# Kernel optimization log

Hardware: AMD Instinct MI355X
Metric: run time of the kernel (lower is better)

Reference implementation:

```python
import jax, jax.numpy as jnp
import numpy as np

B, T, C, H = 8, 2048, 1024, 64

def setup_inputs() -> dict:
    key = jax.random.key(0)
    k1, k2, k3, k4 = jax.random.split(key, 4)
    x = jax.random.normal(k1, (B, T, C), dtype=jnp.float32)
    # torch nn.Linear default init ~ U(-1/sqrt(in), 1/sqrt(in)); scale kept small for stability
    s = 1.0 / np.sqrt(C)
    Wq = jax.random.uniform(k2, (C, H), dtype=jnp.float32, minval=-s, maxval=s)
    Wk = jax.random.uniform(k3, (C, H), dtype=jnp.float32, minval=-s, maxval=s)
    Wv = jax.random.uniform(k4, (C, H), dtype=jnp.float32, minval=-s, maxval=s)
    return {"x": x, "Wq": Wq, "Wk": Wk, "Wv": Wv}

def reference(x, Wq, Wk, Wv):
    # x: [B,T,C]; Wq/Wk/Wv: [C,H] (equivalent to torch Linear weight transposed)
    Q = jnp.einsum('btc,ch->bth', x, Wq)
    K = jnp.einsum('btc,ch->bth', x, Wk)
    V = jnp.einsum('btc,ch->bth', x, Wv)
    H_ = Q.shape[-1]
    scale = 1.0 / jnp.sqrt(jnp.asarray(H_, dtype=Q.dtype))
    w = jnp.einsum('bqh,bkh->bqk', Q, K) * scale  # [B,T,T]
    T_ = x.shape[1]
    causal = jnp.tril(jnp.ones((T_, T_), dtype=bool))
    w = jnp.where(causal, w, -jnp.inf)
    w = jax.nn.softmax(w, axis=-1)
    out = jnp.einsum('bqk,bkh->bqh', w, V)  # [B,T,H]
    return out
```

## Files before the change

### kernel.cpp

```cpp
#include <hip/hip_runtime.h>
#include <math.h>

#define Bb 8
#define Tt 2048
#define Cc 1024
#define Hh 64
#define BT (Bb * Tt)
#define SLOG2E 0.18033688011112042f

typedef __attribute__((ext_vector_type(8))) short short8;
typedef __attribute__((ext_vector_type(4))) float floatx4;

__device__ inline unsigned short f2bf(float f) {
  unsigned int u = __builtin_bit_cast(unsigned int, f);
  u += 0x7fff + ((u >> 16) & 1);
  return (unsigned short)(u >> 16);
}
__device__ inline float bf2f(unsigned short u) {
  unsigned int x = ((unsigned int)u) << 16;
  return __builtin_bit_cast(float, x);
}


__global__ __launch_bounds__(256) void wconv2(
    const float* __restrict__ Wq, const float* __restrict__ Wk,
    const float* __restrict__ Wv, unsigned short* __restrict__ WTf) {
  int bid = blockIdx.x;
  int w = bid >> 5;
  int kc = bid & 31;
  const float* __restrict__ W = (w == 0) ? Wq : (w == 1 ? Wk : Wv);
  int t = threadIdx.x;
  int hg = t >> 6, quad = (t >> 4) & 3, lrow = t & 15;
  int g = w * 4 + hg;
  int h = hg * 16 + lrow;
  unsigned short tmp[8];
#pragma unroll
  for (int j = 0; j < 8; ++j)
    tmp[j] = f2bf(W[(size_t)(kc * 32 + quad * 8 + j) * Hh + h]);
  unsigned short* dst = &WTf[((size_t)(g * 32 + kc) * 64 + quad * 16 + lrow) * 8];
  *(ushort4*)dst = make_ushort4(tmp[0], tmp[1], tmp[2], tmp[3]);
  *(ushort4*)(dst + 4) = make_ushort4(tmp[4], tmp[5], tmp[6], tmp[7]);
}

__global__ __launch_bounds__(256) void qkv7(
    const float* __restrict__ x, const unsigned short* __restrict__ WTf,
    unsigned short* __restrict__ Qf, unsigned short* __restrict__ Kf,
    unsigned short* __restrict__ Vf) {
  __shared__ __align__(16) unsigned short smem7[6656];

  int mt = blockIdx.x;
  int t = threadIdx.x;
  int wv = t >> 6, lane = t & 63;
  int lrow = lane & 15, quad = lane >> 4;

  floatx4 acc[2][3];
#pragma unroll
  for (int g2 = 0; g2 < 2; ++g2)
#pragma unroll
    for (int j = 0; j < 3; ++j)
#pragma unroll
      for (int r = 0; r < 4; ++r) acc[g2][j][r] = 0.f;

  int srow = t >> 3, scg = t & 7;
  int skc2 = scg >> 2, squad = scg & 3;
  int sslot = ((srow >> 4) * 2 + skc2) * 64 + squad * 16 +
              (((srow & 15) + squad + 4 * skc2) & 15);
  const float* xp = x + (size_t)(mt * 32 + srow) * Cc + scg * 8;

  int aslot[2][2];
#pragma unroll
  for (int g2 = 0; g2 < 2; ++g2)
#pragma unroll
    for (int kc2 = 0; kc2 < 2; ++kc2)
      aslot[g2][kc2] = ((g2 * 2 + kc2) * 64 + quad * 16 +
                        ((lrow + quad + 4 * kc2) & 15)) * 8;

  const unsigned short* wbase[3];
#pragma unroll
  for (int j = 0; j < 3; ++j)
    wbase[j] = WTf + (size_t)(wv * 3 + j) * 32 * 512 + lane * 8;

  {
    float4 v0 = *(const float4*)xp;
    float4 v1 = *(const float4*)(xp + 4);
    short8 a;
    a[0] = (short)f2bf(v0.x); a[1] = (short)f2bf(v0.y);
    a[2] = (short)f2bf(v0.z); a[3] = (short)f2bf(v0.w);
    a[4] = (short)f2bf(v1.x); a[5] = (short)f2bf(v1.y);
    a[6] = (short)f2bf(v1.z); a[7] = (short)f2bf(v1.w);
    *(short8*)&smem7[sslot * 8] = a;
  }
  __syncthreads();

  for (int kk = 0; kk < 16; ++kk) {
    int cur = kk & 1;
    float4 v0, v1;
    if (kk < 15) {
      v0 = *(const float4*)(xp + (kk + 1) * 64);
      v1 = *(const float4*)(xp + (kk + 1) * 64 + 4);
    }
    short8 bf[3][2];
    int kg = kk * 2;
#pragma unroll
    for (int j = 0; j < 3; ++j)
#pragma unroll
      for (int kc2 = 0; kc2 < 2; ++kc2)
        bf[j][kc2] = *(const short8*)(wbase[j] + (size_t)(kg + kc2) * 512);
    short8 af[2][2];
#pragma unroll
    for (int g2 = 0; g2 < 2; ++g2)
#pragma unroll
      for (int kc2 = 0; kc2 < 2; ++kc2)
        af[g2][kc2] = *(const short8*)&smem7[cur * 2048 + aslot[g2][kc2]];
#pragma unroll
    for (int g2 = 0; g2 < 2; ++g2)
#pragma unroll
      for (int j = 0; j < 3; ++j) {
        acc[g2][j] = __builtin_amdgcn_mfma_f32_16x16x32_bf16(af[g2][0], bf[j][0], acc[g2][j], 0, 0, 0);
        acc[g2][j] = __builtin_amdgcn_mfma_f32_16x16x32_bf16(af[g2][1], bf[j][1], acc[g2][j], 0, 0, 0);
      }
    if (kk < 15) {
      short8 a;
      a[0] = (short)f2bf(v0.x); a[1] = (short)f2bf(v0.y);
      a[2] = (short)f2bf(v0.z); a[3] = (short)f2bf(v0.w);
      a[4] = (short)f2bf(v1.x); a[5] = (short)f2bf(v1.y);
      a[6] = (short)f2bf(v1.z); a[7] = (short)f2bf(v1.w);
      *(short8*)&smem7[(1 - cur) * 2048 + sslot * 8] = a;
      __syncthreads();
    }
  }

  __syncthreads();
#pragma unroll
  for (int g2 = 0; g2 < 2; ++g2)
#pragma unroll
    for (int j = 0; j < 3; ++j) {
      int col = (wv * 3 + j) * 16 + lrow;
#pragma unroll
      for (int r = 0; r < 4; ++r)
        smem7[(g2 * 16 + quad * 4 + r) * 208 + col] = f2bf(acc[g2][j][r]);
    }
  __syncthreads();
#pragma unroll
  for (int fi = 0; fi < 3; ++fi) {
    int idx = fi * 256 + t;
    if (idx < 512) {
      int which = idx >> 8;
      int sub = idx & 255;
      int g2k = sub >> 6, lane_s = sub & 63;
      int g2_ = g2k >> 1, kc_ = g2k & 1;
      int tokrow = g2_ * 16 + (lane_s & 15);
      int hbase = which * 64 + kc_ * 32 + (lane_s >> 4) * 8;
      short8 v = *(const short8*)&smem7[tokrow * 208 + hbase];
      unsigned short* dstf = which ? Kf : Qf;
      *(short8*)&dstf[((size_t)(mt * 2 + g2_) * 2 + kc_) * 512 + lane_s * 8] = v;
    } else {
      int sub = idx - 512;
      int hs = sub >> 6, lane_s = sub & 63;
      int hcol = 128 + hs * 16 + (lane_s & 15);
      int tok0 = (lane_s >> 4) * 8;
      unsigned short tmp[8];
#pragma unroll
      for (int jj = 0; jj < 8; ++jj) tmp[jj] = smem7[(tok0 + jj) * 208 + hcol];
      unsigned short* dv = &Vf[((size_t)(mt * 4 + hs)) * 512 + lane_s * 8];
      *(ushort4*)dv = make_ushort4(tmp[0], tmp[1], tmp[2], tmp[3]);
      *(ushort4*)(dv + 4) = make_ushort4(tmp[4], tmp[5], tmp[6], tmp[7]);
    }
  }
}

__global__ __launch_bounds__(512) void attn6(
    const unsigned short* __restrict__ Qf, const unsigned short* __restrict__ Kf,
    const unsigned short* __restrict__ Vf, float* __restrict__ out) {
  __shared__ __align__(16) unsigned char smem[33 * 1024];
  unsigned short* Pall = (unsigned short*)smem;
  unsigned short* Ocomb = (unsigned short*)smem;
  float* Lcomb = (float*)(smem + 32768);

  int bid = blockIdx.x;
  int b = bid >> 5;
  int j = bid & 31;
  int t = threadIdx.x;
  int wv = t >> 6, lane = t & 63;
  int lrow = lane & 15, quad = lane >> 4;

  unsigned short* Pw = Pall + wv * 2048;

  short8 ones;
#pragma unroll
  for (int i = 0; i < 8; ++i) ones[i] = (short)0x3F80;

  for (int half = 0; half < 2; ++half) {
    int qt = half ? (63 - j) : j;
    int q0 = qt * 32;
    int nkt = (qt >> 1) + 1;
    int qtile16 = b * 128 + qt * 2;

    short8 aq[2][2];
#pragma unroll
    for (int qs = 0; qs < 2; ++qs)
#pragma unroll
      for (int kc = 0; kc < 2; ++kc)
        aq[qs][kc] = *(const short8*)
            &Qf[((size_t)(qtile16 + qs) * 2 + kc) * 512 + lane * 8];

    floatx4 acc_o[2][4];
    floatx4 acc_l[2];
#pragma unroll
    for (int qs = 0; qs < 2; ++qs) {
#pragma unroll
      for (int r = 0; r < 4; ++r) acc_l[qs][r] = 0.f;
#pragma unroll
      for (int hs = 0; hs < 4; ++hs)
#pragma unroll
        for (int r = 0; r < 4; ++r) acc_o[qs][hs][r] = 0.f;
    }

    for (int kt = wv; kt < nkt; kt += 8) {
      int ktile16 = b * 128 + kt * 4;
      int ktile32 = b * 64 + kt * 2;
      short8 kf[4][2], vf[4][2];
#pragma unroll
      for (int sn = 0; sn < 4; ++sn)
#pragma unroll
        for (int kc = 0; kc < 2; ++kc)
          kf[sn][kc] = *(const short8*)
              &Kf[((size_t)(ktile16 + sn) * 2 + kc) * 512 + lane * 8];
#pragma unroll
      for (int hs = 0; hs < 4; ++hs)
#pragma unroll
        for (int kc = 0; kc < 2; ++kc)
          vf[hs][kc] = *(const short8*)
              &Vf[((size_t)(ktile32 + kc) * 4 + hs) * 512 + lane * 8];

      floatx4 s[2][4];
#pragma unroll
      for (int qs = 0; qs < 2; ++qs)
#pragma unroll
        for (int sn = 0; sn < 4; ++sn) {
          floatx4 z;
#pragma unroll
          for (int r = 0; r < 4; ++r) z[r] = 0.f;
          z = __builtin_amdgcn_mfma_f32_16x16x32_bf16(aq[qs][0], kf[sn][0], z, 0, 0, 0);
          z = __builtin_amdgcn_mfma_f32_16x16x32_bf16(aq[qs][1], kf[sn][1], z, 0, 0, 0);
          s[qs][sn] = z;
        }

      bool diag = (kt == nkt - 1);
#pragma unroll
      for (int qs = 0; qs < 2; ++qs)
#pragma unroll
        for (int sn = 0; sn < 4; ++sn) {
          int k5 = (sn & 1) * 16 + lrow;
          int slot = qs * 2 + (sn >> 1);
          int rlbase = (k5 >> 3) * 16;
#pragma unroll
          for (int r = 0; r < 4; ++r) {
            float v = s[qs][sn][r] * SLOG2E;
            if (diag) {
              int gk = kt * 64 + sn * 16 + lrow;
              int gq = q0 + qs * 16 + quad * 4 + r;
              if (gk > gq) v = -INFINITY;
            }
            float p = exp2f(v);
            Pw[slot * 512 + (rlbase + quad * 4 + r) * 8 + (k5 & 7)] = f2bf(p);
          }
        }

      short8 ap[2][2];
#pragma unroll
      for (int qs = 0; qs < 2; ++qs)
#pragma unroll
        for (int kc = 0; kc < 2; ++kc)
          ap[qs][kc] = *(const short8*)&Pw[(qs * 2 + kc) * 512 + lane * 8];

#pragma unroll
      for (int qs = 0; qs < 2; ++qs) {
        acc_l[qs] = __builtin_amdgcn_mfma_f32_16x16x32_bf16(ap[qs][0], ones, acc_l[qs], 0, 0, 0);
        acc_l[qs] = __builtin_amdgcn_mfma_f32_16x16x32_bf16(ap[qs][1], ones, acc_l[qs], 0, 0, 0);
#pragma unroll
        for (int hs = 0; hs < 4; ++hs) {
          acc_o[qs][hs] = __builtin_amdgcn_mfma_f32_16x16x32_bf16(ap[qs][0], vf[hs][0], acc_o[qs][hs], 0, 0, 0);
          acc_o[qs][hs] = __builtin_amdgcn_mfma_f32_16x16x32_bf16(ap[qs][1], vf[hs][1], acc_o[qs][hs], 0, 0, 0);
        }
      }
    }

#pragma unroll
    for (int qs = 0; qs < 2; ++qs)
#pragma unroll
      for (int hs = 0; hs < 4; ++hs) {
        int s8 = qs * 4 + hs;
        *(ushort4*)&Ocomb[((wv * 8 + s8) * 64 + lane) * 4] =
            make_ushort4(f2bf(acc_o[qs][hs][0]), f2bf(acc_o[qs][hs][1]),
                         f2bf(acc_o[qs][hs][2]), f2bf(acc_o[qs][hs][3]));
      }
    if (lrow == 0) {
#pragma unroll
      for (int qs = 0; qs < 2; ++qs)
#pragma unroll
        for (int r = 0; r < 4; ++r)
          Lcomb[wv * 32 + qs * 16 + quad * 4 + r] = acc_l[qs][r];
    }
    __syncthreads();

    {
      int qsub = wv >> 2, hs = wv & 3;
      float o[4] = {0.f, 0.f, 0.f, 0.f};
#pragma unroll
      for (int w = 0; w < 8; ++w) {
        ushort4 pk = *(const ushort4*)&Ocomb[((w * 8 + wv) * 64 + lane) * 4];
        o[0] += bf2f(pk.x); o[1] += bf2f(pk.y);
        o[2] += bf2f(pk.z); o[3] += bf2f(pk.w);
      }
#pragma unroll
      for (int r = 0; r < 4; ++r) {
        float lv = 0.f;
#pragma unroll
        for (int w = 0; w < 8; ++w)
          lv += Lcomb[w * 32 + qsub * 16 + quad * 4 + r];
        int row = q0 + qsub * 16 + quad * 4 + r;
        out[(size_t)(b * Tt + row) * Hh + hs * 16 + lrow] = o[r] / lv;
      }
    }
    __syncthreads();
  }
}

extern "C" void kernel_launch(void* const* d_in, const int* in_sizes, int n_in,
                              void* d_out, int out_size, void* d_ws, size_t ws_size,
                              hipStream_t stream) {
  const float* x = (const float*)d_in[0];
  const float* Wq = (const float*)d_in[1];
  const float* Wk = (const float*)d_in[2];
  const float* Wv = (const float*)d_in[3];
  float* out = (float*)d_out;

  unsigned short* WTf = (unsigned short*)d_ws;
  unsigned short* Qf = WTf + 192 * 1024;
  unsigned short* Kf = Qf + (size_t)(BT / 16) * 2 * 512;
  unsigned short* Vf = Kf + (size_t)(BT / 16) * 2 * 512;

  wconv2<<<dim3(96), dim3(256), 0, stream>>>(Wq, Wk, Wv, WTf);
  qkv7<<<dim3(512), dim3(256), 0, stream>>>(x, WTf, Qf, Kf, Vf);
  attn6<<<dim3(256), dim3(512), 0, stream>>>(Qf, Kf, Vf, out);
}
```

Baseline: 132.4 us.

## Fuse weight conversion, QKV projection and attention into one cooperative kernel

Replaces three separate kernel launches with a single cooperative kernel that uses grid-wide syncs between weight conversion, QKV projection and attention. The projection stage is retiled to 64 tokens per 512-thread block so 256 blocks cover the work. The intent is to remove launch gaps and tail effects between the stages. In exchange it adds the cost of grid.sync and requires all 256 blocks to be co-resident; the old three-launch path is kept as a fallback if the cooperative launch fails.

```diff
diff --git a/kernel.cpp b/kernel.cpp
--- a/kernel.cpp
+++ b/kernel.cpp
@@ -1,5 +1,8 @@
 #include <hip/hip_runtime.h>
+#include <hip/hip_cooperative_groups.h>
 #include <math.h>
+
+namespace cg = cooperative_groups;
 
 #define Bb 8
 #define Tt 2048
@@ -21,6 +24,318 @@
   return __builtin_bit_cast(float, x);
 }
 
+
+__global__ __launch_bounds__(512) void fused(
+    const float* __restrict__ x,
+    const float* __restrict__ Wq, const float* __restrict__ Wk,
+    const float* __restrict__ Wv,
+    unsigned short* __restrict__ WTf,
+    unsigned short* __restrict__ Qf, unsigned short* __restrict__ Kf,
+    unsigned short* __restrict__ Vf, float* __restrict__ out) {
+  __shared__ __align__(16) unsigned char smemF[34304];
+  cg::grid_group grid = cg::this_grid();
+
+  int bid = blockIdx.x;
+  int t = threadIdx.x;
+  int wv = t >> 6, lane = t & 63;
+  int lrow = lane & 15, quad = lane >> 4;
+
+  if (bid < 48) {
+    int unit = bid * 2 + (t >> 8);
+    int tt = t & 255;
+    int w = unit >> 5;
+    int kc = unit & 31;
+    const float* __restrict__ W = (w == 0) ? Wq : (w == 1 ? Wk : Wv);
+    int hg = tt >> 6, q_ = (tt >> 4) & 3, lr_ = tt & 15;
+    int g = w * 4 + hg;
+    int h = hg * 16 + lr_;
+    unsigned short tmp[8];
+#pragma unroll
+    for (int j = 0; j < 8; ++j)
+      tmp[j] = f2bf(W[(size_t)(kc * 32 + q_ * 8 + j) * Hh + h]);
+    unsigned short* dst = &WTf[((size_t)(g * 32 + kc) * 64 + q_ * 16 + lr_) * 8];
+    *(ushort4*)dst = make_ushort4(tmp[0], tmp[1], tmp[2], tmp[3]);
+    *(ushort4*)(dst + 4) = make_ushort4(tmp[4], tmp[5], tmp[6], tmp[7]);
+  }
+  grid.sync();
+
+  {
+    unsigned short* Af = (unsigned short*)smemF;
+    int mt = bid;
+    int wm = wv & 1;
+    int wq = wv >> 1;
+
+    floatx4 acc[2][3];
+#pragma unroll
+    for (int i = 0; i < 2; ++i)
+#pragma unroll
+      for (int j = 0; j < 3; ++j)
+#pragma unroll
+        for (int r = 0; r < 4; ++r) acc[i][j][r] = 0.f;
+
+    int srow = t >> 3, scg = t & 7;
+    int skc2 = scg >> 2, squad = scg & 3;
+    int sslot = ((srow >> 4) * 2 + skc2) * 512 +
+                (squad * 16 + (((srow & 15) + squad + 4 * skc2) & 15)) * 8;
+    const float* xp = x + (size_t)(mt * 64 + srow) * Cc + scg * 8;
+
+    int aslot[2][2];
+#pragma unroll
+    for (int i = 0; i < 2; ++i)
+#pragma unroll
+      for (int kc2 = 0; kc2 < 2; ++kc2) {
+        int ms = wm * 2 + i;
+        aslot[i][kc2] = ((ms * 2 + kc2) * 512 +
+                         (quad * 16 + ((lrow + quad + 4 * kc2) & 15)) * 8);
+      }
+
+    const unsigned short* wbase[3];
+#pragma unroll
+    for (int j = 0; j < 3; ++j)
+      wbase[j] = WTf + (size_t)(wq * 3 + j) * 32 * 512 + lane * 8;
+
+    {
+      float4 v0 = *(const float4*)xp;
+      float4 v1 = *(const float4*)(xp + 4);
+      short8 a;
+      a[0] = (short)f2bf(v0.x); a[1] = (short)f2bf(v0.y);
+      a[2] = (short)f2bf(v0.z); a[3] = (short)f2bf(v0.w);
+      a[4] = (short)f2bf(v1.x); a[5] = (short)f2bf(v1.y);
+      a[6] = (short)f2bf(v1.z); a[7] = (short)f2bf(v1.w);
+      *(short8*)&Af[sslot] = a;
+    }
+    __syncthreads();
+
+    for (int kk = 0; kk < 16; ++kk) {
+      int cur = kk & 1;
+      float4 v0, v1;
+      if (kk < 15) {
+        v0 = *(const float4*)(xp + (kk + 1) * 64);
+        v1 = *(const float4*)(xp + (kk + 1) * 64 + 4);
+      }
+      short8 bfr[3][2];
+      int kg = kk * 2;
+#pragma unroll
+      for (int j = 0; j < 3; ++j)
+#pragma unroll
+        for (int kc2 = 0; kc2 < 2; ++kc2)
+          bfr[j][kc2] = *(const short8*)(wbase[j] + (size_t)(kg + kc2) * 512);
+      short8 af[2][2];
+#pragma unroll
+      for (int i = 0; i < 2; ++i)
+#pragma unroll
+        for (int kc2 = 0; kc2 < 2; ++kc2)
+          af[i][kc2] = *(const short8*)&Af[cur * 4096 + aslot[i][kc2]];
+#pragma unroll
+      for (int i = 0; i < 2; ++i)
+#pragma unroll
+        for (int j = 0; j < 3; ++j) {
+          acc[i][j] = __builtin_amdgcn_mfma_f32_16x16x32_bf16(af[i][0], bfr[j][0], acc[i][j], 0, 0, 0);
+          acc[i][j] = __builtin_amdgcn_mfma_f32_16x16x32_bf16(af[i][1], bfr[j][1], acc[i][j], 0, 0, 0);
+        }
+      if (kk < 15) {
+        short8 a;
+        a[0] = (short)f2bf(v0.x); a[1] = (short)f2bf(v0.y);
+        a[2] = (short)f2bf(v0.z); a[3] = (short)f2bf(v0.w);
+        a[4] = (short)f2bf(v1.x); a[5] = (short)f2bf(v1.y);
+        a[6] = (short)f2bf(v1.z); a[7] = (short)f2bf(v1.w);
+        *(short8*)&Af[(1 - cur) * 4096 + sslot] = a;
+        __syncthreads();
+      }
+    }
+
+    __syncthreads();
+    unsigned short* Dt = (unsigned short*)smemF;
+#pragma unroll
+    for (int i = 0; i < 2; ++i)
+#pragma unroll
+      for (int j = 0; j < 3; ++j) {
+        int col = (wq * 3 + j) * 16 + lrow;
+        int rowb = (wm * 2 + i) * 16 + quad * 4;
+#pragma unroll
+        for (int r = 0; r < 4; ++r)
+          Dt[(rowb + r) * 208 + col] = f2bf(acc[i][j][r]);
+      }
+    __syncthreads();
+#pragma unroll
+    for (int fi = 0; fi < 3; ++fi) {
+      int idx = fi * 512 + t;
+      int tile = idx >> 6, lane_s = idx & 63;
+      if (tile < 16) {
+        int which = tile >> 3;
+        int sub = tile & 7;
+        int g2 = sub >> 1, kc = sub & 1;
+        int tokrow = g2 * 16 + (lane_s & 15);
+        int hbase = which * 64 + kc * 32 + (lane_s >> 4) * 8;
+        short8 v = *(const short8*)&Dt[tokrow * 208 + hbase];
+        unsigned short* dstf = which ? Kf : Qf;
+        *(short8*)&dstf[((size_t)(mt * 4 + g2) * 2 + kc) * 512 + lane_s * 8] = v;
+      } else {
+        int sub = tile - 16;
+        int t32 = sub >> 2, hs = sub & 3;
+        int hcol = 128 + hs * 16 + (lane_s & 15);
+        int tok0 = t32 * 32 + (lane_s >> 4) * 8;
+        unsigned short tmp[8];
+#pragma unroll
+        for (int jj = 0; jj < 8; ++jj) tmp[jj] = Dt[(tok0 + jj) * 208 + hcol];
+        unsigned short* dv = &Vf[((size_t)(mt * 2 + t32) * 4 + hs) * 512 + lane_s * 8];
+        *(ushort4*)dv = make_ushort4(tmp[0], tmp[1], tmp[2], tmp[3]);
+        *(ushort4*)(dv + 4) = make_ushort4(tmp[4], tmp[5], tmp[6], tmp[7]);
+      }
+    }
+  }
+  grid.sync();
+
+  {
+    unsigned short* Pall = (unsigned short*)smemF;
+    unsigned short* Ocomb = (unsigned short*)smemF;
+    float* Lcomb = (float*)(smemF + 32768);
+    unsigned short* Pw = Pall + wv * 2048;
+
+    int b = bid >> 5;
+    int j = bid & 31;
+
+    short8 ones;
+#pragma unroll
+    for (int i = 0; i < 8; ++i) ones[i] = (short)0x3F80;
+
+    for (int half = 0; half < 2; ++half) {
+      int qt = half ? (63 - j) : j;
+      int q0 = qt * 32;
+      int nkt = (qt >> 1) + 1;
+      int qtile16 = b * 128 + qt * 2;
+
+      short8 aq[2][2];
+#pragma unroll
+      for (int qs = 0; qs < 2; ++qs)
+#pragma unroll
+        for (int kc = 0; kc < 2; ++kc)
+          aq[qs][kc] = *(const short8*)
+              &Qf[((size_t)(qtile16 + qs) * 2 + kc) * 512 + lane * 8];
+
+      floatx4 acc_o[2][4];
+      floatx4 acc_l[2];
+#pragma unroll
+      for (int qs = 0; qs < 2; ++qs) {
+#pragma unroll
+        for (int r = 0; r < 4; ++r) acc_l[qs][r] = 0.f;
+#pragma unroll
+        for (int hs = 0; hs < 4; ++hs)
+#pragma unroll
+          for (int r = 0; r < 4; ++r) acc_o[qs][hs][r] = 0.f;
+      }
+
+      for (int kt = wv; kt < nkt; kt += 8) {
+        int ktile16 = b * 128 + kt * 4;
+        int ktile32 = b * 64 + kt * 2;
+        short8 kf[4][2], vf[4][2];
+#pragma unroll
+        for (int sn = 0; sn < 4; ++sn)
+#pragma unroll
+          for (int kc = 0; kc < 2; ++kc)
+            kf[sn][kc] = *(const short8*)
+                &Kf[((size_t)(ktile16 + sn) * 2 + kc) * 512 + lane * 8];
+#pragma unroll
+        for (int hs = 0; hs < 4; ++hs)
+#pragma unroll
+          for (int kc = 0; kc < 2; ++kc)
+            vf[hs][kc] = *(const short8*)
+                &Vf[((size_t)(ktile32 + kc) * 4 + hs) * 512 + lane * 8];
+
+        floatx4 s[2][4];
+#pragma unroll
+        for (int qs = 0; qs < 2; ++qs)
+#pragma unroll
+          for (int sn = 0; sn < 4; ++sn) {
+            floatx4 z;
+#pragma unroll
+            for (int r = 0; r < 4; ++r) z[r] = 0.f;
+            z = __builtin_amdgcn_mfma_f32_16x16x32_bf16(aq[qs][0], kf[sn][0], z, 0, 0, 0);
+            z = __builtin_amdgcn_mfma_f32_16x16x32_bf16(aq[qs][1], kf[sn][1], z, 0, 0, 0);
+            s[qs][sn] = z;
+          }
+
+        bool diag = (kt == nkt - 1);
+#pragma unroll
+        for (int qs = 0; qs < 2; ++qs)
+#pragma unroll
+          for (int sn = 0; sn < 4; ++sn) {
+            int k5 = (sn & 1) * 16 + lrow;
+            int slot = qs * 2 + (sn >> 1);
+            int rlbase = (k5 >> 3) * 16;
+#pragma unroll
+            for (int r = 0; r < 4; ++r) {
+              float v = s[qs][sn][r] * SLOG2E;
+              if (diag) {
+                int gk = kt * 64 + sn * 16 + lrow;
+                int gq = q0 + qs * 16 + quad * 4 + r;
+                if (gk > gq) v = -INFINITY;
+              }
+              float p = exp2f(v);
+              Pw[slot * 512 + (rlbase + quad * 4 + r) * 8 + (k5 & 7)] = f2bf(p);
+            }
+          }
+
+        short8 ap[2][2];
+#pragma unroll
+        for (int qs = 0; qs < 2; ++qs)
+#pragma unroll
+          for (int kc = 0; kc < 2; ++kc)
+            ap[qs][kc] = *(const short8*)&Pw[(qs * 2 + kc) * 512 + lane * 8];
+
+#pragma unroll
+        for (int qs = 0; qs < 2; ++qs) {
+          acc_l[qs] = __builtin_amdgcn_mfma_f32_16x16x32_bf16(ap[qs][0], ones, acc_l[qs], 0, 0, 0);
+          acc_l[qs] = __builtin_amdgcn_mfma_f32_16x16x32_bf16(ap[qs][1], ones, acc_l[qs], 0, 0, 0);
+#pragma unroll
+          for (int hs = 0; hs < 4; ++hs) {
+            acc_o[qs][hs] = __builtin_amdgcn_mfma_f32_16x16x32_bf16(ap[qs][0], vf[hs][0], acc_o[qs][hs], 0, 0, 0);
+            acc_o[qs][hs] = __builtin_amdgcn_mfma_f32_16x16x32_bf16(ap[qs][1], vf[hs][1], acc_o[qs][hs], 0, 0, 0);
+          }
+        }
+      }
+
+#pragma unroll
+      for (int qs = 0; qs < 2; ++qs)
+#pragma unroll
+        for (int hs = 0; hs < 4; ++hs) {
+          int s8 = qs * 4 + hs;
+          *(ushort4*)&Ocomb[((wv * 8 + s8) * 64 + lane) * 4] =
+              make_ushort4(f2bf(acc_o[qs][hs][0]), f2bf(acc_o[qs][hs][1]),
+                           f2bf(acc_o[qs][hs][2]), f2bf(acc_o[qs][hs][3]));
+        }
+      if (lrow == 0) {
+#pragma unroll
+        for (int qs = 0; qs < 2; ++qs)
+#pragma unroll
+          for (int r = 0; r < 4; ++r)
+            Lcomb[wv * 32 + qs * 16 + quad * 4 + r] = acc_l[qs][r];
+      }
+      __syncthreads();
+
+      {
+        int qsub = wv >> 2, hs = wv & 3;
+        float o[4] = {0.f, 0.f, 0.f, 0.f};
+#pragma unroll
+        for (int w = 0; w < 8; ++w) {
+          ushort4 pk = *(const ushort4*)&Ocomb[((w * 8 + wv) * 64 + lane) * 4];
+          o[0] += bf2f(pk.x); o[1] += bf2f(pk.y);
+          o[2] += bf2f(pk.z); o[3] += bf2f(pk.w);
+        }
+#pragma unroll
+        for (int r = 0; r < 4; ++r) {
+          float lv = 0.f;
+#pragma unroll
+          for (int w = 0; w < 8; ++w)
+            lv += Lcomb[w * 32 + qsub * 16 + quad * 4 + r];
+          int row = q0 + qsub * 16 + quad * 4 + r;
+          out[(size_t)(b * Tt + row) * Hh + hs * 16 + lrow] = o[r] / lv;
+        }
+      }
+      __syncthreads();
+    }
+  }
+}
 
 __global__ __launch_bounds__(256) void wconv2(
     const float* __restrict__ Wq, const float* __restrict__ Wk,
@@ -47,12 +362,10 @@
     unsigned short* __restrict__ Qf, unsigned short* __restrict__ Kf,
     unsigned short* __restrict__ Vf) {
   __shared__ __align__(16) unsigned short smem7[6656];
-
   int mt = blockIdx.x;
   int t = threadIdx.x;
   int wv = t >> 6, lane = t & 63;
   int lrow = lane & 15, quad = lane >> 4;
-
   floatx4 acc[2][3];
 #pragma unroll
   for (int g2 = 0; g2 < 2; ++g2)
@@ -60,13 +373,11 @@
     for (int j = 0; j < 3; ++j)
 #pragma unroll
       for (int r = 0; r < 4; ++r) acc[g2][j][r] = 0.f;
-
   int srow = t >> 3, scg = t & 7;
   int skc2 = scg >> 2, squad = scg & 3;
   int sslot = ((srow >> 4) * 2 + skc2) * 64 + squad * 16 +
               (((srow & 15) + squad + 4 * skc2) & 15);
   const float* xp = x + (size_t)(mt * 32 + srow) * Cc + scg * 8;
-
   int aslot[2][2];
 #pragma unroll
   for (int g2 = 0; g2 < 2; ++g2)
@@ -74,12 +385,10 @@
     for (int kc2 = 0; kc2 < 2; ++kc2)
       aslot[g2][kc2] = ((g2 * 2 + kc2) * 64 + quad * 16 +
                         ((lrow + quad + 4 * kc2) & 15)) * 8;
-
   const unsigned short* wbase[3];
 #pragma unroll
   for (int j = 0; j < 3; ++j)
     wbase[j] = WTf + (size_t)(wv * 3 + j) * 32 * 512 + lane * 8;
-
   {
     float4 v0 = *(const float4*)xp;
     float4 v1 = *(const float4*)(xp + 4);
@@ -91,7 +400,6 @@
     *(short8*)&smem7[sslot * 8] = a;
   }
   __syncthreads();
-
   for (int kk = 0; kk < 16; ++kk) {
     int cur = kk & 1;
     float4 v0, v1;
@@ -99,13 +407,13 @@
       v0 = *(const float4*)(xp + (kk + 1) * 64);
       v1 = *(const float4*)(xp + (kk + 1) * 64 + 4);
     }
-    short8 bf[3][2];
+    short8 bfr[3][2];
     int kg = kk * 2;
 #pragma unroll
     for (int j = 0; j < 3; ++j)
 #pragma unroll
       for (int kc2 = 0; kc2 < 2; ++kc2)
-        bf[j][kc2] = *(const short8*)(wbase[j] + (size_t)(kg + kc2) * 512);
+        bfr[j][kc2] = *(const short8*)(wbase[j] + (size_t)(kg + kc2) * 512);
     short8 af[2][2];
 #pragma unroll
     for (int g2 = 0; g2 < 2; ++g2)
@@ -116,8 +424,8 @@
     for (int g2 = 0; g2 < 2; ++g2)
 #pragma unroll
       for (int j = 0; j < 3; ++j) {
-        acc[g2][j] = __builtin_amdgcn_mfma_f32_16x16x32_bf16(af[g2][0], bf[j][0], acc[g2][j], 0, 0, 0);
-        acc[g2][j] = __builtin_amdgcn_mfma_f32_16x16x32_bf16(af[g2][1], bf[j][1], acc[g2][j], 0, 0, 0);
+        acc[g2][j] = __builtin_amdgcn_mfma_f32_16x16x32_bf16(af[g2][0], bfr[j][0], acc[g2][j], 0, 0, 0);
+        acc[g2][j] = __builtin_amdgcn_mfma_f32_16x16x32_bf16(af[g2][1], bfr[j][1], acc[g2][j], 0, 0, 0);
       }
     if (kk < 15) {
       short8 a;
@@ -129,7 +437,6 @@
       __syncthreads();
     }
   }
-
   __syncthreads();
 #pragma unroll
   for (int g2 = 0; g2 < 2; ++g2)
@@ -176,26 +483,21 @@
   unsigned short* Pall = (unsigned short*)smem;
   unsigned short* Ocomb = (unsigned short*)smem;
   float* Lcomb = (float*)(smem + 32768);
-
   int bid = blockIdx.x;
   int b = bid >> 5;
   int j = bid & 31;
   int t = threadIdx.x;
   int wv = t >> 6, lane = t & 63;
   int lrow = lane & 15, quad = lane >> 4;
-
   unsigned short* Pw = Pall + wv * 2048;
-
   short8 ones;
 #pragma unroll
   for (int i = 0; i < 8; ++i) ones[i] = (short)0x3F80;
-
   for (int half = 0; half < 2; ++half) {
     int qt = half ? (63 - j) : j;
     int q0 = qt * 32;
     int nkt = (qt >> 1) + 1;
     int qtile16 = b * 128 + qt * 2;
-
     short8 aq[2][2];
 #pragma unroll
     for (int qs = 0; qs < 2; ++qs)
@@ -203,7 +505,6 @@
       for (int kc = 0; kc < 2; ++kc)
         aq[qs][kc] = *(const short8*)
             &Qf[((size_t)(qtile16 + qs) * 2 + kc) * 512 + lane * 8];
-
     floatx4 acc_o[2][4];
     floatx4 acc_l[2];
 #pragma unroll
@@ -215,7 +516,6 @@
 #pragma unroll
         for (int r = 0; r < 4; ++r) acc_o[qs][hs][r] = 0.f;
     }
-
     for (int kt = wv; kt < nkt; kt += 8) {
       int ktile16 = b * 128 + kt * 4;
       int ktile32 = b * 64 + kt * 2;
@@ -232,7 +532,6 @@
         for (int kc = 0; kc < 2; ++kc)
           vf[hs][kc] = *(const short8*)
               &Vf[((size_t)(ktile32 + kc) * 4 + hs) * 512 + lane * 8];
-
       floatx4 s[2][4];
 #pragma unroll
       for (int qs = 0; qs < 2; ++qs)
@@ -245,7 +544,6 @@
           z = __builtin_amdgcn_mfma_f32_16x16x32_bf16(aq[qs][1], kf[sn][1], z, 0, 0, 0);
           s[qs][sn] = z;
         }
-
       bool diag = (kt == nkt - 1);
 #pragma unroll
       for (int qs = 0; qs < 2; ++qs)
@@ -266,14 +564,12 @@
             Pw[slot * 512 + (rlbase + quad * 4 + r) * 8 + (k5 & 7)] = f2bf(p);
           }
         }
-
       short8 ap[2][2];
 #pragma unroll
       for (int qs = 0; qs < 2; ++qs)
 #pragma unroll
         for (int kc = 0; kc < 2; ++kc)
           ap[qs][kc] = *(const short8*)&Pw[(qs * 2 + kc) * 512 + lane * 8];
-
 #pragma unroll
       for (int qs = 0; qs < 2; ++qs) {
         acc_l[qs] = __builtin_amdgcn_mfma_f32_16x16x32_bf16(ap[qs][0], ones, acc_l[qs], 0, 0, 0);
@@ -285,7 +581,6 @@
         }
       }
     }
-
 #pragma unroll
     for (int qs = 0; qs < 2; ++qs)
 #pragma unroll
@@ -303,7 +598,6 @@
           Lcomb[wv * 32 + qs * 16 + quad * 4 + r] = acc_l[qs][r];
     }
     __syncthreads();
-
     {
       int qsub = wv >> 2, hs = wv & 3;
       float o[4] = {0.f, 0.f, 0.f, 0.f};
@@ -341,7 +635,14 @@
   unsigned short* Kf = Qf + (size_t)(BT / 16) * 2 * 512;
   unsigned short* Vf = Kf + (size_t)(BT / 16) * 2 * 512;
 
-  wconv2<<<dim3(96), dim3(256), 0, stream>>>(Wq, Wk, Wv, WTf);
-  qkv7<<<dim3(512), dim3(256), 0, stream>>>(x, WTf, Qf, Kf, Vf);
-  attn6<<<dim3(256), dim3(512), 0, stream>>>(Qf, Kf, Vf, out);
+  void* kargs[] = {(void*)&x, (void*)&Wq, (void*)&Wk, (void*)&Wv,
+                   (void*)&WTf, (void*)&Qf, (void*)&Kf, (void*)&Vf,
+                   (void*)&out};
+  hipError_t ce = hipLaunchCooperativeKernel((const void*)fused, dim3(256),
+                                             dim3(512), kargs, 0, stream);
+  if (ce != hipSuccess) {
+    wconv2<<<dim3(96), dim3(256), 0, stream>>>(Wq, Wk, Wv, WTf);
+    qkv7<<<dim3(512), dim3(256), 0, stream>>>(x, WTf, Qf, Kf, Vf);
+    attn6<<<dim3(256), dim3(512), 0, stream>>>(Qf, Kf, Vf, out);
+  }
 }
```

Result: slower. 198.1 us (+49.7%).
